# Kernel optimization log

Measured on AMD Instinct MI355X. Metric: run time of the kernel, lower is better.

The kernel has to match this reference:

```python
import jax, jax.numpy as jnp
import numpy as np

T, B, NMUL = 730, 1000, 8
NEARZERO = 1e-5
LENF = 15
A_LO, A_HI = 0.1, 1.0
B_LO, B_HI = 50.0, 500.0
C_LO, C_HI = 0.0, 1.0
D_LO, D_HI = 0.01, 0.9
RA_LO, RA_HI = 0.0, 2.9
RB_LO, RB_HI = 0.0, 6.5
S_INIT, G_INIT = 50.0, 10.0


def setup_inputs() -> dict:
    key = jax.random.key(0)
    k1, k2 = jax.random.split(key)
    # forcing: prcp in [0,10) mm/day, pet in [0,5) mm/day
    x = jax.random.uniform(k1, (T, B, 2), dtype=jnp.float32) * jnp.array([10.0, 5.0], dtype=jnp.float32)
    # NN-produced raw params in [0,1): 4*NMUL physical + 2 routing
    raw_phy_static = jax.random.uniform(k2, (B, 4 * NMUL + 2), dtype=jnp.float32)
    return {"x": x, "raw_phy_static": raw_phy_static}


def _descale(p, lo, hi):
    return p * (hi - lo) + lo


def _uh_gamma(rout_a, rout_b):
    # gamma-distribution unit hydrograph, (B,) params -> (B, LENF) kernel
    aa = jax.nn.relu(rout_a)[:, None] + 0.1      # shape parameter
    theta = jax.nn.relu(rout_b)[:, None] + 0.5   # scale parameter
    t = jnp.arange(0.5, LENF, 1.0, dtype=jnp.float32)[None, :]  # midpoints 0.5..14.5
    logw = (aa - 1.0) * jnp.log(t) - t / theta - jax.scipy.special.gammaln(aa) - aa * jnp.log(theta)
    w = jnp.exp(logw)
    return w / w.sum(1, keepdims=True)


def _uh_conv(q, UH):
    # causal per-basin convolution: y[b,t] = sum_k q[b,t-k]*UH[b,k]; q (B,T), UH (B,LENF)
    n = q.shape[1]
    conv1 = lambda qb, wb: jnp.convolve(qb, wb, mode='full')[:n]
    return jax.vmap(conv1)(q, UH)


def reference(x, raw_phy_static):
    phy = raw_phy_static[:, :4 * NMUL].reshape(B, 4, NMUL)  # (B,4,NMUL)
    a = _descale(phy[:, 0], A_LO, A_HI)
    b = _descale(phy[:, 1], B_LO, B_HI)
    c = _descale(phy[:, 2], C_LO, C_HI)
    d = _descale(phy[:, 3], D_LO, D_HI)
    rout_a = _descale(raw_phy_static[:, 4 * NMUL], RA_LO, RA_HI)  # (B,)
    rout_b = _descale(raw_phy_static[:, 4 * NMUL + 1], RB_LO, RB_HI)

    ones_mul = jnp.ones((1, 1, NMUL), dtype=x.dtype)
    P = x[:, :, 0:1] * ones_mul    # (T,B,NMUL)
    PET = x[:, :, 1:2] * ones_mul  # (T,B,NMUL)

    S0 = jnp.full((B, NMUL), S_INIT, dtype=x.dtype)
    G0 = jnp.full((B, NMUL), G_INIT, dtype=x.dtype)

    def step(carry, inp):
        S, G = carry
        p, pet = inp
        W = p + S                                   # available water
        term = (W + b) / (2.0 * a)
        Y = term - jnp.sqrt(jnp.maximum(term * term - W * b / a, NEARZERO))  # ET opportunity
        S_new = Y * jnp.exp(-pet / b)               # soil storage
        AET = Y - S_new                             # actual ET
        avail = W - Y                               # water available for runoff/recharge
        Qsurf = (1.0 - c) * avail                   # direct runoff
        G_new = (G + c * avail) / (1.0 + d)         # groundwater storage
        Qgw = d * G_new                             # baseflow
        Qsim = Qsurf + Qgw
        return (S_new, G_new), (Qsim, Qsurf, Qgw, AET, S_new, G_new, W, Y)

    (_, _), (Qsim, Qsurf, Qgw, AET, Sout, Gout, Wout, Yout) = jax.lax.scan(step, (S0, G0), (P, PET))

    UH = _uh_gamma(rout_a, rout_b)                  # (B,LENF)
    Qs = _uh_conv(Qsim.mean(-1).T, UH).T[..., None]        # routed streamflow (T,B,1)
    Qsurf_r = _uh_conv(Qsurf.mean(-1).T, UH).T[..., None]  # routed surface runoff
    Qgw_r = _uh_conv(Qgw.mean(-1).T, UH).T[..., None]      # routed groundwater flow

    out = jnp.concatenate([
        Qs, Qsurf_r, Qgw_r,
        AET.mean(-1, keepdims=True),
        Sout.mean(-1, keepdims=True),
        Gout.mean(-1, keepdims=True),
    ], axis=-1)  # (T,B,6)
    return out
```

## Files before the change

kernel.cpp:

```cpp
#include <hip/hip_runtime.h>
#include <math.h>

#define T_STEPS 730
#define NB      1000
#define LENF    15
#define NEARZ   1e-5f
#define TPAD    736
#define NLANES  8000

#define STEPA(CURV, Q, SIDX)                                                   \
  {                                                                            \
    float pcp = (CURV).x, pet = (CURV).y;                                      \
    float W     = pcp + S;                                                     \
    float term  = fmaf(W, inv2a, pb2a);                                        \
    float disc  = fmaf(term, term, -(W * boa));                                \
    float r     = __builtin_amdgcn_sqrtf(fmaxf(disc, NEARZ));                  \
    float Y     = term - r;                                                    \
    float e     = __builtin_amdgcn_exp2f(pet * ninvbl2);                       \
    float Sn    = Y * e;                                                       \
    float avail = W - Y;                                                       \
    float Gn    = fmaf(pc, avail, G) * inv1pd;                                 \
    S = Sn; G = Gn;                                                            \
    sr[(Q)] = Sn;                                                              \
    gr[(Q)] = Gn;                                                              \
    if (((Q) & 3) == 3) {                                                      \
      *(float4*)(pS + (SIDX) - 3) =                                            \
          make_float4(sr[(Q) - 3], sr[(Q) - 2], sr[(Q) - 1], sr[(Q)]);         \
      *(float4*)(pG + (SIDX) - 3) =                                            \
          make_float4(gr[(Q) - 3], gr[(Q) - 2], gr[(Q) - 1], gr[(Q)]);         \
    }                                                                          \
  }

#define PREFETCH(BUF, CI)                                                      \
  _Pragma("unroll")                                                            \
  for (int j = 0; j < 8; ++j) {                                                \
      int tt = (CI) * 8 + j;                                                   \
      tt = tt < T_STEPS ? tt : (T_STEPS - 1);                                  \
      BUF[j] = xf[tt * NB + b];                                                \
  }                                                                            \
  __builtin_amdgcn_sched_barrier(0);

__global__ __launch_bounds__(64, 1) void scan_state(const float* __restrict__ x,
                                                    const float* __restrict__ raw,
                                                    float* __restrict__ snp,
                                                    float* __restrict__ gnp) {
    const int L   = threadIdx.x;
    const int gid = blockIdx.x * 64 + L;
    const int b   = gid >> 3;
    const int m   = gid & 7;

    const float* rp = raw + b * 34;
    float pa = rp[0 * 8 + m] * 0.9f + 0.1f;
    float pb = rp[1 * 8 + m] * 450.0f + 50.0f;
    float pc = rp[2 * 8 + m];
    float pd = rp[3 * 8 + m] * 0.89f + 0.01f;

    float inv2a   = 1.0f / (2.0f * pa);
    float pb2a    = pb * inv2a;
    float boa     = pb / pa;
    float ninvbl2 = -1.4426950408889634f / pb;
    float inv1pd  = 1.0f / (1.0f + pd);

    float* pS = snp + (size_t)gid * TPAD;
    float* pG = gnp + (size_t)gid * TPAD;

    float S = 50.0f, G = 10.0f;
    float sr[16], gr[16];

    const float2* __restrict__ xf = (const float2*)x;

    float2 A[8], Bb[8], Cc[8];
    PREFETCH(A, 0)
    PREFETCH(Bb, 1)

    for (int g = 0; g < 15; ++g) {
        const int c0 = 6 * g;
        PREFETCH(Cc, c0 + 2)
#pragma unroll
        for (int j = 0; j < 8; ++j) STEPA(A[j],  j,      j)
        PREFETCH(A, c0 + 3)
#pragma unroll
        for (int j = 0; j < 8; ++j) STEPA(Bb[j], 8 + j,  8 + j)
        PREFETCH(Bb, c0 + 4)
#pragma unroll
        for (int j = 0; j < 8; ++j) STEPA(Cc[j], j,      16 + j)
        PREFETCH(Cc, c0 + 5)
#pragma unroll
        for (int j = 0; j < 8; ++j) STEPA(A[j],  8 + j,  24 + j)
        PREFETCH(A, c0 + 6)
#pragma unroll
        for (int j = 0; j < 8; ++j) STEPA(Bb[j], j,      32 + j)
        PREFETCH(Bb, c0 + 7)
#pragma unroll
        for (int j = 0; j < 8; ++j) STEPA(Cc[j], 8 + j,  40 + j)
        pS += 48; pG += 48;
    }
#pragma unroll
    for (int j = 0; j < 8; ++j) STEPA(A[j], j, j)
    STEPA(Bb[0], 8, 8)
    STEPA(Bb[1], 9, 9)
    *(float2*)(pS + 8) = make_float2(sr[8], sr[9]);
    *(float2*)(pG + 8) = make_float2(gr[8], gr[9]);
}

__global__ __launch_bounds__(256) void finalize(const float* __restrict__ x,
                                                const float* __restrict__ raw,
                                                const float* __restrict__ snp,
                                                const float* __restrict__ gnp,
                                                float* __restrict__ out) {
    __shared__ float qs_sh[270], qg_sh[270];

    const int b     = blockIdx.y;
    const int tbase = blockIdx.x * 256;
    const int tid   = threadIdx.x;

    const float* rp = raw + b * 34;
    float e2s[8], omc_[8], d_[8];
#pragma unroll
    for (int m = 0; m < 8; ++m) {
        float pb = rp[8 + m] * 450.0f + 50.0f;
        e2s[m]  = 1.4426950408889634f / pb;
        omc_[m] = 1.0f - rp[16 + m];
        d_[m]   = rp[24 + m] * 0.89f + 0.01f;
    }

    const float2* __restrict__ xf = (const float2*)x;

#pragma unroll
    for (int it = 0; it < 2; ++it) {
        int idx = tid + it * 256;
        if (idx < 270) {
            int tt = tbase + idx - 14;
            float qs = 0.0f, qg = 0.0f;
            if (tt >= 0 && tt < T_STEPS) {
                float2 pc2 = xf[tt * NB + b];
                float p = pc2.x, pet = pc2.y;
                float aet = 0.0f, ssum = 0.0f, gsum = 0.0f;
                int tprev = tt > 0 ? tt - 1 : 0;
#pragma unroll
                for (int m = 0; m < 8; ++m) {
                    const float* rowS = snp + (size_t)(b * 8 + m) * TPAD;
                    const float* rowG = gnp + (size_t)(b * 8 + m) * TPAD;
                    float sn = rowS[tt];
                    float sp = tt > 0 ? rowS[tprev] : 50.0f;
                    float gn = rowG[tt];
                    float y  = sn * __builtin_amdgcn_exp2f(pet * e2s[m]);
                    float avail = (p + sp) - y;
                    qs   += omc_[m] * avail;
                    qg   += d_[m] * gn;
                    aet  += y - sn;
                    ssum += sn;
                    gsum += gn;
                }
                if (idx >= 14) {
                    float* o = out + ((size_t)tt * NB + b) * 6;
                    o[3] = aet * 0.125f;
                    o[4] = ssum * 0.125f;
                    o[5] = gsum * 0.125f;
                }
            }
            qs_sh[idx] = qs;
            qg_sh[idx] = qg;
        }
    }
    __syncthreads();

    const int t = tbase + tid;
    if (t >= T_STEPS) return;

    float ra = rp[32] * 2.9f;
    float rb = rp[33] * 6.5f;
    float aa = fmaxf(ra, 0.0f) + 0.1f;
    float th = fmaxf(rb, 0.0f) + 0.5f;
    float inv_th = 1.0f / th;
    float am1 = aa - 1.0f;
    float w[LENF];
    float sw = 0.0f;
#pragma unroll
    for (int k = 0; k < LENF; ++k) {
        float tk = (float)k + 0.5f;
        w[k] = __expf(am1 * __logf(tk) - tk * inv_th);
        sw += w[k];
    }
    float invs = 0.125f / sw;
    float ys = 0.0f, yg = 0.0f;
#pragma unroll
    for (int k = 0; k < LENF; ++k) {
        float wk = w[k] * invs;
        ys = fmaf(qs_sh[tid + 14 - k], wk, ys);
        yg = fmaf(qg_sh[tid + 14 - k], wk, yg);
    }
    float* o = out + ((size_t)t * NB + b) * 6;
    o[0] = ys + yg;
    o[1] = ys;
    o[2] = yg;
}

template <int CTRL>
__device__ __forceinline__ float dpp_mov(float x) {
    int xi = __builtin_bit_cast(int, x);
    int r  = __builtin_amdgcn_update_dpp(0, xi, CTRL, 0xF, 0xF, true);
    return __builtin_bit_cast(float, r);
}
__device__ __forceinline__ float sum8(float v) {
    v += dpp_mov<0xB1>(v);
    v += dpp_mov<0x4E>(v);
    v += dpp_mov<0x141>(v);
    return v;
}

#define STEPF(CURV)                                                            \
  {                                                                            \
    float pcp = (CURV).x, pet = (CURV).y;                                      \
    float W     = pcp + S;                                                     \
    float term  = fmaf(W, inv2a, pb2a);                                        \
    float disc  = fmaf(term, term, -(W * boa));                                \
    float r     = __builtin_amdgcn_sqrtf(fmaxf(disc, NEARZ));                  \
    float Y     = term - r;                                                    \
    float e     = __builtin_amdgcn_exp2f(pet * ninvbl2);                       \
    float Sn    = Y * e;                                                       \
    float AET   = Y - Sn;                                                      \
    float avail = W - Y;                                                       \
    float Qs    = omc * avail;                                                 \
    float Gn    = fmaf(pc, avail, G) * inv1pd;                                 \
    float Qg    = pd * Gn;                                                     \
    S = Sn; G = Gn;                                                            \
    float qs_s = sum8(Qs);                                                     \
    float qg_s = sum8(Qg);                                                     \
    float ae_s = sum8(AET);                                                    \
    float s_s  = sum8(Sn);                                                     \
    float g_s  = sum8(Gn);                                                     \
    float v = qs_s;                                                            \
    v = (m == 1) ? qg_s : v;                                                   \
    v = (m == 2) ? ae_s : v;                                                   \
    v = (m == 3) ? s_s  : v;                                                   \
    v = (m >= 4) ? g_s  : v;                                                   \
    *optr = v * 0.125f;                                                        \
    optr += incr;                                                              \
  }

__global__ __launch_bounds__(64, 1) void scan_fb(const float* __restrict__ x,
                                                 const float* __restrict__ raw,
                                                 float* __restrict__ out,
                                                 float* __restrict__ qs_ws,
                                                 float* __restrict__ qg_ws,
                                                 float* __restrict__ dummy) {
    const int L  = threadIdx.x;
    const int lb = L >> 3;
    const int m  = L & 7;
    const int b  = blockIdx.x * 8 + lb;

    const float* rp = raw + b * 34;
    float pa = rp[0 * 8 + m] * 0.9f + 0.1f;
    float pb = rp[1 * 8 + m] * 450.0f + 50.0f;
    float pc = rp[2 * 8 + m];
    float pd = rp[3 * 8 + m] * 0.89f + 0.01f;
    float inv2a   = 1.0f / (2.0f * pa);
    float pb2a    = pb * inv2a;
    float boa     = pb / pa;
    float ninvbl2 = -1.4426950408889634f / pb;
    float omc     = 1.0f - pc;
    float inv1pd  = 1.0f / (1.0f + pd);

    float* optr;
    long long incr;
    if      (m == 0) { optr = qs_ws + b;                      incr = NB;     }
    else if (m == 1) { optr = qg_ws + b;                      incr = NB;     }
    else if (m <= 4) { optr = out + (long long)b * 6 + m + 1; incr = NB * 6; }
    else             { optr = dummy + (blockIdx.x * 64 + L);  incr = 0;      }

    float S = 50.0f, G = 10.0f;
    const float2* __restrict__ xf = (const float2*)x;

    float2 A[10], B[10], C[10];
#pragma unroll
    for (int j = 0; j < 10; ++j) A[j] = xf[j * NB + b];
#pragma unroll
    for (int j = 0; j < 10; ++j) B[j] = xf[(10 + j) * NB + b];

    for (int cg = 0; cg < 24; ++cg) {
        const int c0 = 3 * cg;
#pragma unroll
        for (int j = 0; j < 10; ++j) C[j] = xf[((c0 + 2) * 10 + j) * NB + b];
        __builtin_amdgcn_sched_barrier(0);
#pragma unroll
        for (int j = 0; j < 10; ++j) STEPF(A[j]);
#pragma unroll
        for (int j = 0; j < 10; ++j) A[j] = xf[((c0 + 3) * 10 + j) * NB + b];
        __builtin_amdgcn_sched_barrier(0);
#pragma unroll
        for (int j = 0; j < 10; ++j) STEPF(B[j]);
#pragma unroll
        for (int j = 0; j < 10; ++j) {
            int t = (c0 + 4) * 10 + j;
            t = t < T_STEPS ? t : (T_STEPS - 1);
            B[j] = xf[t * NB + b];
        }
        __builtin_amdgcn_sched_barrier(0);
#pragma unroll
        for (int j = 0; j < 10; ++j) STEPF(C[j]);
    }
#pragma unroll
    for (int j = 0; j < 10; ++j) STEPF(A[j]);
}

__global__ __launch_bounds__(256) void uh_fb(const float* __restrict__ raw,
                                             float* __restrict__ uh) {
    int b = blockIdx.x * 256 + threadIdx.x;
    if (b >= NB) return;
    float ra = raw[b * 34 + 32] * 2.9f;
    float rb = raw[b * 34 + 33] * 6.5f;
    float aa = fmaxf(ra, 0.0f) + 0.1f;
    float th = fmaxf(rb, 0.0f) + 0.5f;
    float inv_th = 1.0f / th;
    float am1 = aa - 1.0f;
    float w[LENF];
    float s = 0.0f;
#pragma unroll
    for (int k = 0; k < LENF; ++k) {
        float t = (float)k + 0.5f;
        w[k] = __expf(am1 * __logf(t) - t * inv_th);
        s += w[k];
    }
    float invs = 1.0f / s;
#pragma unroll
    for (int k = 0; k < LENF; ++k) uh[k * NB + b] = w[k] * invs;
}

__global__ __launch_bounds__(256) void conv_fb(const float* __restrict__ qs_ws,
                                               const float* __restrict__ qg_ws,
                                               const float* __restrict__ uh,
                                               float* __restrict__ out) {
    int b = blockIdx.x * 256 + threadIdx.x;
    int t = blockIdx.y;
    if (b >= NB) return;
    float ys = 0.0f, yg = 0.0f;
    int kmax = t < (LENF - 1) ? t : (LENF - 1);
    for (int k = 0; k <= kmax; ++k) {
        float w = uh[k * NB + b];
        ys = fmaf(qs_ws[(t - k) * NB + b], w, ys);
        yg = fmaf(qg_ws[(t - k) * NB + b], w, yg);
    }
    float* o = out + (t * NB + b) * 6;
    o[0] = ys + yg;
    o[1] = ys;
    o[2] = yg;
}

extern "C" void kernel_launch(void* const* d_in, const int* in_sizes, int n_in,
                              void* d_out, int out_size, void* d_ws, size_t ws_size,
                              hipStream_t stream) {
    const float* x   = (const float*)d_in[0];
    const float* raw = (const float*)d_in[1];
    float* out = (float*)d_out;

    const size_t need = (size_t)NLANES * TPAD * 2 * sizeof(float);
    if (ws_size >= need) {
        float* snp = (float*)d_ws;
        float* gnp = snp + (size_t)NLANES * TPAD;
        scan_state<<<dim3(NLANES / 64), dim3(64),  0, stream>>>(x, raw, snp, gnp);
        finalize  <<<dim3(3, NB),       dim3(256), 0, stream>>>(x, raw, snp, gnp, out);
    } else {
        float* qs = (float*)d_ws;
        float* qg = qs + (size_t)T_STEPS * NB;
        float* uh = qg + (size_t)T_STEPS * NB;
        float* dm = uh + (size_t)LENF * NB;
        uh_fb  <<<dim3((NB + 255) / 256),          dim3(256), 0, stream>>>(raw, uh);
        scan_fb<<<dim3(NB / 8),                    dim3(64),  0, stream>>>(x, raw, out, qs, qg, dm);
        conv_fb<<<dim3((NB + 255) / 256, T_STEPS), dim3(256), 0, stream>>>(qs, qg, uh, out);
    }
}
```

Measured before the change: 126.3 us.

## Store scan state time-major as interleaved float2 and retile finalize over basins

The scan kernel now writes S and G together as one float2 per lane per timestep, laid out time-major, so the 64 lanes of a wave write adjacent addresses. Before, each lane wrote float4 runs along its own padded row. The finalize kernel is rebuilt around 32-timestep by 32-basin tiles: each thread handles one (basin, multiplier) lane, the 8 multipliers are reduced with DPP, the results go to a padded shared-memory tile, and the routing convolution reads from that tile. This is meant to give coalesced loads and stores in both kernels. The cost is a serial loop over timesteps inside finalize, a 14-step halo recomputed per tile, and scattered 4-byte output stores.

```diff
diff --git a/kernel.cpp b/kernel.cpp
--- a/kernel.cpp
+++ b/kernel.cpp
@@ -5,10 +5,11 @@
 #define NB      1000
 #define LENF    15
 #define NEARZ   1e-5f
-#define TPAD    736
-#define NLANES  8000
-
-#define STEPA(CURV, Q, SIDX)                                                   \
+#define SGW     8000
+#define TT      32
+#define BBLK    32
+
+#define STEPA(CURV)                                                            \
   {                                                                            \
     float pcp = (CURV).x, pet = (CURV).y;                                      \
     float W     = pcp + S;                                                     \
@@ -16,19 +17,13 @@
     float disc  = fmaf(term, term, -(W * boa));                                \
     float r     = __builtin_amdgcn_sqrtf(fmaxf(disc, NEARZ));                  \
     float Y     = term - r;                                                    \
-    float e     = __builtin_amdgcn_exp2f(pet * ninvbl2);                       \
+    float e     = __builtin_amdgcn_exp2f(pet * nbl);                           \
     float Sn    = Y * e;                                                       \
     float avail = W - Y;                                                       \
-    float Gn    = fmaf(pc, avail, G) * inv1pd;                                 \
+    float Gn    = fmaf(pc, avail, G) * i1d;                                    \
     S = Sn; G = Gn;                                                            \
-    sr[(Q)] = Sn;                                                              \
-    gr[(Q)] = Gn;                                                              \
-    if (((Q) & 3) == 3) {                                                      \
-      *(float4*)(pS + (SIDX) - 3) =                                            \
-          make_float4(sr[(Q) - 3], sr[(Q) - 2], sr[(Q) - 1], sr[(Q)]);         \
-      *(float4*)(pG + (SIDX) - 3) =                                            \
-          make_float4(gr[(Q) - 3], gr[(Q) - 2], gr[(Q) - 1], gr[(Q)]);         \
-    }                                                                          \
+    *psg = make_float2(Sn, Gn);                                                \
+    psg += SGW;                                                                \
   }
 
 #define PREFETCH(BUF, CI)                                                      \
@@ -42,8 +37,7 @@
 
 __global__ __launch_bounds__(64, 1) void scan_state(const float* __restrict__ x,
                                                     const float* __restrict__ raw,
-                                                    float* __restrict__ snp,
-                                                    float* __restrict__ gnp) {
+                                                    float2* __restrict__ sg) {
     const int L   = threadIdx.x;
     const int gid = blockIdx.x * 64 + L;
     const int b   = gid >> 3;
@@ -55,17 +49,14 @@
     float pc = rp[2 * 8 + m];
     float pd = rp[3 * 8 + m] * 0.89f + 0.01f;
 
-    float inv2a   = 1.0f / (2.0f * pa);
-    float pb2a    = pb * inv2a;
-    float boa     = pb / pa;
-    float ninvbl2 = -1.4426950408889634f / pb;
-    float inv1pd  = 1.0f / (1.0f + pd);
-
-    float* pS = snp + (size_t)gid * TPAD;
-    float* pG = gnp + (size_t)gid * TPAD;
+    float inv2a = 1.0f / (2.0f * pa);
+    float pb2a  = pb * inv2a;
+    float boa   = pb / pa;
+    float nbl   = -1.4426950408889634f / pb;
+    float i1d   = 1.0f / (1.0f + pd);
 
     float S = 50.0f, G = 10.0f;
-    float sr[16], gr[16];
+    float2* psg = sg + gid;
 
     const float2* __restrict__ xf = (const float2*)x;
 
@@ -77,99 +68,117 @@
         const int c0 = 6 * g;
         PREFETCH(Cc, c0 + 2)
 #pragma unroll
-        for (int j = 0; j < 8; ++j) STEPA(A[j],  j,      j)
+        for (int j = 0; j < 8; ++j) STEPA(A[j])
         PREFETCH(A, c0 + 3)
 #pragma unroll
-        for (int j = 0; j < 8; ++j) STEPA(Bb[j], 8 + j,  8 + j)
+        for (int j = 0; j < 8; ++j) STEPA(Bb[j])
         PREFETCH(Bb, c0 + 4)
 #pragma unroll
-        for (int j = 0; j < 8; ++j) STEPA(Cc[j], j,      16 + j)
+        for (int j = 0; j < 8; ++j) STEPA(Cc[j])
         PREFETCH(Cc, c0 + 5)
 #pragma unroll
-        for (int j = 0; j < 8; ++j) STEPA(A[j],  8 + j,  24 + j)
+        for (int j = 0; j < 8; ++j) STEPA(A[j])
         PREFETCH(A, c0 + 6)
 #pragma unroll
-        for (int j = 0; j < 8; ++j) STEPA(Bb[j], j,      32 + j)
+        for (int j = 0; j < 8; ++j) STEPA(Bb[j])
         PREFETCH(Bb, c0 + 7)
 #pragma unroll
-        for (int j = 0; j < 8; ++j) STEPA(Cc[j], 8 + j,  40 + j)
-        pS += 48; pG += 48;
-    }
-#pragma unroll
-    for (int j = 0; j < 8; ++j) STEPA(A[j], j, j)
-    STEPA(Bb[0], 8, 8)
-    STEPA(Bb[1], 9, 9)
-    *(float2*)(pS + 8) = make_float2(sr[8], sr[9]);
-    *(float2*)(pG + 8) = make_float2(gr[8], gr[9]);
+        for (int j = 0; j < 8; ++j) STEPA(Cc[j])
+    }
+#pragma unroll
+    for (int j = 0; j < 8; ++j) STEPA(A[j])
+    STEPA(Bb[0])
+    STEPA(Bb[1])
+}
+
+template <int CTRL>
+__device__ __forceinline__ float dpp_mov(float x) {
+    int xi = __builtin_bit_cast(int, x);
+    int r  = __builtin_amdgcn_update_dpp(0, xi, CTRL, 0xF, 0xF, true);
+    return __builtin_bit_cast(float, r);
+}
+__device__ __forceinline__ float sum8(float v) {
+    v += dpp_mov<0xB1>(v);
+    v += dpp_mov<0x4E>(v);
+    v += dpp_mov<0x141>(v);
+    return v;
 }
 
 __global__ __launch_bounds__(256) void finalize(const float* __restrict__ x,
                                                 const float* __restrict__ raw,
-                                                const float* __restrict__ snp,
-                                                const float* __restrict__ gnp,
+                                                const float2* __restrict__ sg,
                                                 float* __restrict__ out) {
-    __shared__ float qs_sh[270], qg_sh[270];
-
-    const int b     = blockIdx.y;
-    const int tbase = blockIdx.x * 256;
+    __shared__ float qsh[TT + 14][BBLK + 1];
+    __shared__ float qgh[TT + 14][BBLK + 1];
+
     const int tid   = threadIdx.x;
-
-    const float* rp = raw + b * 34;
-    float e2s[8], omc_[8], d_[8];
-#pragma unroll
-    for (int m = 0; m < 8; ++m) {
-        float pb = rp[8 + m] * 450.0f + 50.0f;
-        e2s[m]  = 1.4426950408889634f / pb;
-        omc_[m] = 1.0f - rp[16 + m];
-        d_[m]   = rp[24 + m] * 0.89f + 0.01f;
-    }
+    const int lb    = tid >> 3;
+    const int m     = tid & 7;
+    const int tbase = blockIdx.x * TT;
+    const int b0    = blockIdx.y * BBLK;
+    const int b     = b0 + lb;
+    const bool bval = b < NB;
+    const int bc    = bval ? b : (NB - 1);
+    const int lane  = bc * 8 + m;
+
+    const float* rp = raw + bc * 34;
+    float pbm = rp[8 + m] * 450.0f + 50.0f;
+    float e2s = 1.4426950408889634f / pbm;
+    float omc = 1.0f - rp[16 + m];
+    float dm  = rp[24 + m] * 0.89f + 0.01f;
 
     const float2* __restrict__ xf = (const float2*)x;
 
-#pragma unroll
-    for (int it = 0; it < 2; ++it) {
-        int idx = tid + it * 256;
-        if (idx < 270) {
-            int tt = tbase + idx - 14;
-            float qs = 0.0f, qg = 0.0f;
-            if (tt >= 0 && tt < T_STEPS) {
-                float2 pc2 = xf[tt * NB + b];
-                float p = pc2.x, pet = pc2.y;
-                float aet = 0.0f, ssum = 0.0f, gsum = 0.0f;
-                int tprev = tt > 0 ? tt - 1 : 0;
-#pragma unroll
-                for (int m = 0; m < 8; ++m) {
-                    const float* rowS = snp + (size_t)(b * 8 + m) * TPAD;
-                    const float* rowG = gnp + (size_t)(b * 8 + m) * TPAD;
-                    float sn = rowS[tt];
-                    float sp = tt > 0 ? rowS[tprev] : 50.0f;
-                    float gn = rowG[tt];
-                    float y  = sn * __builtin_amdgcn_exp2f(pet * e2s[m]);
-                    float avail = (p + sp) - y;
-                    qs   += omc_[m] * avail;
-                    qg   += d_[m] * gn;
-                    aet  += y - sn;
-                    ssum += sn;
-                    gsum += gn;
-                }
-                if (idx >= 14) {
-                    float* o = out + ((size_t)tt * NB + b) * 6;
-                    o[3] = aet * 0.125f;
-                    o[4] = ssum * 0.125f;
-                    o[5] = gsum * 0.125f;
-                }
+    float Sprev = 50.0f;
+    int tt0  = tbase - 14;
+    int ttc0 = tt0 < 0 ? 0 : tt0;
+    float2 sgv = sg[(size_t)ttc0 * SGW + lane];
+    float2 pv  = xf[ttc0 * NB + bc];
+
+    for (int r = 0; r < TT + 14; ++r) {
+        const int tt = tbase + r - 14;
+        int ttn = tt + 1;
+        ttn = ttn < 0 ? 0 : (ttn >= T_STEPS ? T_STEPS - 1 : ttn);
+        float2 sgn = sg[(size_t)ttn * SGW + lane];
+        float2 pvn = xf[ttn * NB + bc];
+
+        const bool tval = (tt >= 0) && (tt < T_STEPS);
+        float qs = 0.0f, qg = 0.0f, aet = 0.0f, sX = 0.0f, gX = 0.0f;
+        if (tval) {
+            float sp    = (tt == 0) ? 50.0f : Sprev;
+            float y     = sgv.x * __builtin_amdgcn_exp2f(pv.y * e2s);
+            float avail = (pv.x + sp) - y;
+            qs  = omc * avail;
+            qg  = dm * sgv.y;
+            aet = y - sgv.x;
+            sX  = sgv.x;
+            gX  = sgv.y;
+        }
+        qs = sum8(qs);
+        qg = sum8(qg);
+        if (m == 0) { qsh[r][lb] = qs; qgh[r][lb] = qg; }
+        if (r >= 14 && tval) {
+            float a_s = sum8(aet);
+            float s_s = sum8(sX);
+            float g_s = sum8(gX);
+            if (bval && m < 3) {
+                float v = (m == 0) ? a_s : ((m == 1) ? s_s : g_s);
+                out[((size_t)tt * NB + b) * 6 + 3 + m] = v * 0.125f;
             }
-            qs_sh[idx] = qs;
-            qg_sh[idx] = qg;
         }
+        Sprev = sgv.x;
+        sgv = sgn; pv = pvn;
     }
     __syncthreads();
 
-    const int t = tbase + tid;
-    if (t >= T_STEPS) return;
-
-    float ra = rp[32] * 2.9f;
-    float rb = rp[33] * 6.5f;
+    const int bl2 = tid & 31;
+    const int tl0 = tid >> 5;
+    const int b2  = b0 + bl2;
+    if (b2 >= NB) return;
+
+    const float* rp2 = raw + b2 * 34;
+    float ra = rp2[32] * 2.9f;
+    float rb = rp2[33] * 6.5f;
     float aa = fmaxf(ra, 0.0f) + 0.1f;
     float th = fmaxf(rb, 0.0f) + 0.5f;
     float inv_th = 1.0f / th;
@@ -183,30 +192,26 @@
         sw += w[k];
     }
     float invs = 0.125f / sw;
-    float ys = 0.0f, yg = 0.0f;
-#pragma unroll
-    for (int k = 0; k < LENF; ++k) {
-        float wk = w[k] * invs;
-        ys = fmaf(qs_sh[tid + 14 - k], wk, ys);
-        yg = fmaf(qg_sh[tid + 14 - k], wk, yg);
-    }
-    float* o = out + ((size_t)t * NB + b) * 6;
-    o[0] = ys + yg;
-    o[1] = ys;
-    o[2] = yg;
-}
-
-template <int CTRL>
-__device__ __forceinline__ float dpp_mov(float x) {
-    int xi = __builtin_bit_cast(int, x);
-    int r  = __builtin_amdgcn_update_dpp(0, xi, CTRL, 0xF, 0xF, true);
-    return __builtin_bit_cast(float, r);
-}
-__device__ __forceinline__ float sum8(float v) {
-    v += dpp_mov<0xB1>(v);
-    v += dpp_mov<0x4E>(v);
-    v += dpp_mov<0x141>(v);
-    return v;
+#pragma unroll
+    for (int k = 0; k < LENF; ++k) w[k] *= invs;
+
+#pragma unroll
+    for (int it = 0; it < 4; ++it) {
+        int tl = tl0 + it * 8;
+        int t  = tbase + tl;
+        if (t < T_STEPS) {
+            float ys = 0.0f, yg = 0.0f;
+#pragma unroll
+            for (int k = 0; k < LENF; ++k) {
+                ys = fmaf(qsh[tl + 14 - k][bl2], w[k], ys);
+                yg = fmaf(qgh[tl + 14 - k][bl2], w[k], yg);
+            }
+            float* o = out + ((size_t)t * NB + b2) * 6;
+            o[0] = ys + yg;
+            o[1] = ys;
+            o[2] = yg;
+        }
+    }
 }
 
 #define STEPF(CURV)                                                            \
@@ -354,12 +359,12 @@
     const float* raw = (const float*)d_in[1];
     float* out = (float*)d_out;
 
-    const size_t need = (size_t)NLANES * TPAD * 2 * sizeof(float);
+    const size_t need = (size_t)T_STEPS * SGW * sizeof(float2);
     if (ws_size >= need) {
-        float* snp = (float*)d_ws;
-        float* gnp = snp + (size_t)NLANES * TPAD;
-        scan_state<<<dim3(NLANES / 64), dim3(64),  0, stream>>>(x, raw, snp, gnp);
-        finalize  <<<dim3(3, NB),       dim3(256), 0, stream>>>(x, raw, snp, gnp, out);
+        float2* sg = (float2*)d_ws;
+        scan_state<<<dim3(SGW / 64), dim3(64),  0, stream>>>(x, raw, sg);
+        finalize  <<<dim3((T_STEPS + TT - 1) / TT, (NB + BBLK - 1) / BBLK),
+                     dim3(256), 0, stream>>>(x, raw, sg, out);
     } else {
         float* qs = (float*)d_ws;
         float* qg = qs + (size_t)T_STEPS * NB;
```

New measurement: 123.2 us. 1.03x faster.
